# Kernel optimization log

Measured on AMD Instinct MI355X. Metric: run time of the kernel, lower is better.

## Reference

```python
import jax, jax.numpy as jnp
import numpy as np

EMBED = 1024
HEADS = 16
HEAD_DIM = EMBED // HEADS
WINDOW = 256

def _linear(x, W, b):
    # torch nn.Linear: y = x @ W.T + b, W shape (out, in)
    return jnp.einsum('bse,oe->bso', x, W) + b

def setup_inputs() -> dict:
    key = jax.random.key(0)
    ks = jax.random.split(key, 16)
    B, S = 2, 2048
    std = 1.0 / np.sqrt(EMBED)
    d = {
        'query': jax.random.normal(ks[0], (B, S, EMBED), jnp.float32),
        'key':   jax.random.normal(ks[1], (B, S, EMBED), jnp.float32),
        'value': jax.random.normal(ks[2], (B, S, EMBED), jnp.float32),
        'Wq': jax.random.normal(ks[3], (EMBED, EMBED), jnp.float32) * std,
        'bq': jnp.zeros((EMBED,), jnp.float32),
        'Wk': jax.random.normal(ks[4], (EMBED, EMBED), jnp.float32) * std,
        'bk': jnp.zeros((EMBED,), jnp.float32),
        'Wv': jax.random.normal(ks[5], (EMBED, EMBED), jnp.float32) * std,
        'bv': jnp.zeros((EMBED,), jnp.float32),
        'Wo': jax.random.normal(ks[6], (EMBED, EMBED), jnp.float32) * std,
        'bo': jnp.zeros((EMBED,), jnp.float32),
    }
    return d

def reference(query, key, value, Wq, bq, Wk, bk, Wv, bv, Wo, bo):
    B, S, E = query.shape
    q = _linear(query, Wq, bq)
    k = _linear(key, Wk, bk)
    v = _linear(value, Wv, bv)
    # (B, H, S, D)
    q = q.reshape(B, S, HEADS, HEAD_DIM).transpose(0, 2, 1, 3)
    k = k.reshape(B, S, HEADS, HEAD_DIM).transpose(0, 2, 1, 3)
    v = v.reshape(B, S, HEADS, HEAD_DIM).transpose(0, 2, 1, 3)
    scale = 1.0 / jnp.sqrt(jnp.asarray(HEAD_DIM, q.dtype))
    scores = jnp.einsum('bhqd,bhkd->bhqk', q, k) * scale
    # Faithful local masking: mask is 0 inside window [i-w//2, i+w//2], 1 outside,
    # and is ADDED to scores (as in the source, not -inf fill).
    i = jnp.arange(S)[:, None]
    j = jnp.arange(S)[None, :]
    half = WINDOW // 2
    band = (jnp.abs(i - j) <= half)
    add_mask = jnp.where(band, 0.0, 1.0).astype(scores.dtype)  # (S, S)
    scores = scores + add_mask[None, None, :, :]
    attn = jax.nn.softmax(scores, axis=-1)  # dropout = identity (eval)
    out = jnp.einsum('bhqk,bhkd->bhqd', attn, v)
    out = out.transpose(0, 2, 1, 3).reshape(B, S, E)
    return _linear(out, Wo, bo)
```

## Files before the change

kernel.cpp:

```cpp
#include <hip/hip_runtime.h>
#include <stdint.h>

#define B_ 2
#define S_ 2048
#define E_ 1024
#define H_ 16
#define D_ 64
#define M_ (B_*S_)
#define PROJ_ ((size_t)M_*E_)
#define HALF_W 128

typedef float    f32x4 __attribute__((ext_vector_type(4)));
typedef short    s16x4 __attribute__((ext_vector_type(4)));
typedef short    s16x8 __attribute__((ext_vector_type(8)));
typedef __bf16   bf16x8 __attribute__((ext_vector_type(8)));
typedef _Float16 f16x8 __attribute__((ext_vector_type(8)));
typedef unsigned int u32x4 __attribute__((ext_vector_type(4)));

typedef const __attribute__((address_space(1))) void* gas_t;
typedef __attribute__((address_space(3))) void*       las_t;

__device__ __forceinline__ void gl16(const void* g, void* l) {
    __builtin_amdgcn_global_load_lds((gas_t)g, (las_t)l, 16, 0, 0);
}

__device__ __forceinline__ f32x4 MFMA(bf16x8 a, bf16x8 b, f32x4 c) {
    return __builtin_amdgcn_mfma_f32_16x16x32_bf16(a, b, c, 0, 0, 0);
}
__device__ __forceinline__ f32x4 MFMAH(f16x8 a, f16x8 b, f32x4 c) {
    return __builtin_amdgcn_mfma_f32_16x16x32_f16(a, b, c, 0, 0, 0);
}

__device__ __forceinline__ float fexp2(float x) {
    return __builtin_amdgcn_exp2f(x);
}

__device__ __forceinline__ unsigned short f2bf(float f) {
    union { float f; unsigned int u; } x; x.f = f;
    unsigned int u = x.u + 0x7FFFu + ((x.u >> 16) & 1u);
    return (unsigned short)(u >> 16);
}

__device__ __forceinline__ s16x8 cvt8(f32x4 a, f32x4 b) {
    s16x8 h;
    h[0]=(short)f2bf(a[0]); h[1]=(short)f2bf(a[1]); h[2]=(short)f2bf(a[2]); h[3]=(short)f2bf(a[3]);
    h[4]=(short)f2bf(b[0]); h[5]=(short)f2bf(b[1]); h[6]=(short)f2bf(b[2]); h[7]=(short)f2bf(b[3]);
    return h;
}

__global__ __launch_bounds__(256) void cvt_kernel(
    const float* __restrict__ q, const float* __restrict__ k, const float* __restrict__ v,
    const float* __restrict__ Wq, const float* __restrict__ Wk,
    const float* __restrict__ Wv, const float* __restrict__ Wo,
    unsigned short* __restrict__ xq, unsigned short* __restrict__ xk,
    unsigned short* __restrict__ xv, unsigned short* __restrict__ wbf)
{
    const int z = blockIdx.y;
    if (z >= 3 && blockIdx.x >= 512) return;
    const float* src; unsigned short* dst;
    switch (z) {
        case 0: src = q;  dst = xq; break;
        case 1: src = k;  dst = xk; break;
        case 2: src = v;  dst = xv; break;
        case 3: src = Wq; dst = wbf; break;
        case 4: src = Wk; dst = wbf + (size_t)E_*E_; break;
        case 5: src = Wv; dst = wbf + 2*(size_t)E_*E_; break;
        default: src = Wo; dst = wbf + 3*(size_t)E_*E_; break;
    }
    size_t i = ((size_t)blockIdx.x * 256 + threadIdx.x) * 8;
    f32x4 a = *(const f32x4*)(src + i);
    f32x4 c = *(const f32x4*)(src + i + 4);
    *(s16x8*)(dst + i) = cvt8(a, c);
}

__global__ __launch_bounds__(256, 3) void qkv_kernel(
    const unsigned short* __restrict__ xq, const unsigned short* __restrict__ xk,
    const unsigned short* __restrict__ xv,
    const unsigned short* __restrict__ wbf,
    const float* __restrict__ Wq, const float* __restrict__ Wk, const float* __restrict__ Wv,
    const float* __restrict__ bq, const float* __restrict__ bk, const float* __restrict__ bv,
    unsigned short* __restrict__ qkvout)
{
    const int z = blockIdx.z;
    const unsigned short* X  = (z==0) ? xq : (z==1) ? xk : xv;
    const float*          Wf = (z==0) ? Wq : (z==1) ? Wk : Wv;
    const float*        bias = (z==0) ? bq : (z==1) ? bk : bv;
    const unsigned short* Wb = wbf ? (wbf + (size_t)z * E_ * E_) : nullptr;
    unsigned short* dst = qkvout + (size_t)z * PROJ_;

    __shared__ __align__(16) unsigned short As[2][128 * 32];
    __shared__ __align__(16) unsigned short Bs[2][128 * 32];

    const int t = threadIdx.x;
    const int lane = t & 63, w = t >> 6;
    const int quad = lane >> 4, l16 = lane & 15;
    const int wo = (w & 1) * 64, wsb = (w >> 1) * 64;
    const int oBase = blockIdx.x * 128, sBase = blockIdx.y * 128;

    const int r0 = t >> 2;
    const int c4 = (t & 3) ^ (r0 & 3);
    const unsigned short* gX  = X + (size_t)(sBase + r0) * E_ + c4 * 8;
    const unsigned short* gWb = Wb ? Wb + (size_t)(oBase + r0) * E_ + c4 * 8 : nullptr;
    const float*          gWf = Wf + (size_t)(oBase + r0) * E_ + c4 * 8;

    f32x4 acc[4][4] = {};

    auto issue = [&](int kk, int pb) {
        unsigned short* dB = &Bs[pb][(size_t)w * 512];
        gl16(gX + kk, dB);
        gl16(gX + (size_t)64 * E_ + kk, dB + 2048);
        if (gWb) {
            unsigned short* dA = &As[pb][(size_t)w * 512];
            gl16(gWb + kk, dA);
            gl16(gWb + (size_t)64 * E_ + kk, dA + 2048);
        } else {
            const float* gp0 = gWf + kk;
            const float* gp1 = gWf + (size_t)64 * E_ + kk;
            f32x4 a0 = *(const f32x4*)gp0, a1 = *(const f32x4*)(gp0 + 4);
            f32x4 b0 = *(const f32x4*)gp1, b1 = *(const f32x4*)(gp1 + 4);
            *(s16x8*)&As[pb][(size_t)r0 * 32 + (t & 3) * 8]        = cvt8(a0, a1);
            *(s16x8*)&As[pb][(size_t)(r0 + 64) * 32 + (t & 3) * 8] = cvt8(b0, b1);
        }
    };

    issue(0, 0);
    __syncthreads();

    for (int s = 0; s < 32; s++) {
        const int pb = s & 1;
        if (s < 31) issue((s + 1) * 32, pb ^ 1);

        bf16x8 af[4], bfr[4];
        #pragma unroll
        for (int io = 0; io < 4; io++) {
            int r = wo + io * 16 + l16;
            af[io] = *(const bf16x8*)&As[pb][(size_t)r * 32 + ((quad ^ (l16 & 3)) * 8)];
        }
        #pragma unroll
        for (int is = 0; is < 4; is++) {
            int r = wsb + is * 16 + l16;
            bfr[is] = *(const bf16x8*)&Bs[pb][(size_t)r * 32 + ((quad ^ (l16 & 3)) * 8)];
        }
        #pragma unroll
        for (int io = 0; io < 4; io++)
            #pragma unroll
            for (int is = 0; is < 4; is++)
                acc[io][is] = MFMA(af[io], bfr[is], acc[io][is]);
        __syncthreads();
    }

    const float KSCL = 0.1803368801111204f;
    #pragma unroll
    for (int is = 0; is < 4; is++) {
        int sg = sBase + wsb + is * 16 + l16;
        int b = sg >> 11, sg2 = sg & 2047;
        int k6 = sg2 & 63;
        int slot = ((k6 >> 5) & 1) * 32 + ((k6 >> 2) & 3) * 8
                 + ((k6 >> 4) & 1) * 4 + (k6 & 3);
        #pragma unroll
        for (int io = 0; io < 4; io++) {
            int ocol0 = oBase + wo + io * 16 + quad * 4;
            f32x4 bias4 = *(const f32x4*)&bias[ocol0];
            int h = ocol0 >> 6, d0 = ocol0 & 63;
            size_t base = ((size_t)(b * H_ + h)) * ((size_t)S_ * D_);
            if (z == 0) {
                s16x4 h4;
                #pragma unroll
                for (int r = 0; r < 4; r++) h4[r] = (short)f2bf(acc[io][is][r] + bias4[r]);
                *(s16x4*)&dst[base + (size_t)sg2 * D_ + d0] = h4;
            } else if (z == 1) {
                s16x4 h4;
                #pragma unroll
                for (int r = 0; r < 4; r++)
                    h4[r] = (short)f2bf((acc[io][is][r] + bias4[r]) * KSCL);
                *(s16x4*)&dst[base + (size_t)sg2 * D_ + d0] = h4;
            } else {
                size_t vb = base + (size_t)(sg2 >> 6) * 4096 + (size_t)d0 * 64 + slot;
                #pragma unroll
                for (int r = 0; r < 4; r++) {
                    _Float16 hv = (_Float16)(acc[io][is][r] + bias4[r]);
                    dst[vb + (size_t)r * 64] = __builtin_bit_cast(unsigned short, hv);
                }
            }
        }
    }
}

__global__ __launch_bounds__(256, 4) void attn_kernel(
    const unsigned short* __restrict__ qkvout, unsigned short* __restrict__ attnout)
{
    const int bh = blockIdx.x, b = bh >> 4, h = bh & 15;
    const int qbase = blockIdx.y * 64;
    const int t = threadIdx.x, w = t >> 6, lane = t & 63;
    const int quad = lane >> 4, l16 = lane & 15;

    const unsigned short* qg = qkvout + (size_t)bh * (S_ * D_);
    const unsigned short* kg = qkvout + PROJ_ + (size_t)bh * (S_ * D_);
    const unsigned short* vT = qkvout + 2 * PROJ_ + (size_t)bh * (S_ * D_);

    __shared__ __align__(16) unsigned short Ks [2][64 * 64];
    __shared__ __align__(16) unsigned short VTs[2][64 * 64];

    const int qi = qbase + w * 16 + l16;
    bf16x8 aq0 = *(const bf16x8*)&qg[(size_t)qi * 64 + quad * 8];
    bf16x8 aq1 = *(const bf16x8*)&qg[(size_t)qi * 64 + 32 + quad * 8];

    f32x4 Oi[4] = {}, Oo[4] = {};
    f32x4 Si = {}, So = {};

    const int r0 = t >> 3;
    const int ch = ((t & 7) ^ (r0 & 7)) * 8;

    f16x8 onesv;
    #pragma unroll
    for (int j = 0; j < 8; j++) onesv[j] = (_Float16)1.0f;

    auto issue = [&](int kt, int pb) {
        unsigned short* dK = &Ks [pb][(size_t)w * 512];
        unsigned short* dV = &VTs[pb][(size_t)w * 512];
        gl16(kg + (size_t)(kt + r0) * 64 + ch,      dK);
        gl16(kg + (size_t)(kt + r0 + 32) * 64 + ch, dK + 2048);
        gl16(vT + (size_t)(kt + r0) * 64 + ch,      dV);
        gl16(vT + (size_t)(kt + r0 + 32) * 64 + ch, dV + 2048);
    };

    issue(0, 0);
    __syncthreads();

    #pragma unroll 2
    for (int s = 0; s < 32; s++) {
        const int pb = s & 1;
        const int kt = s * 64;
        if (s < 31) issue(kt + 64, pb ^ 1);

        const int dq = qbase - kt;
        const int adq = dq < 0 ? -dq : dq;
        const int cls = (adq <= 64) ? 0 : (adq >= 192 ? 1 : 2);

        f32x4 pp[4];
        const int sw = l16 & 7;
        #pragma unroll
        for (int sub = 0; sub < 4; sub++) {
            int row = sub * 16 + l16;
            bf16x8 bk0 = *(const bf16x8*)&Ks[pb][(size_t)row * 64 + ((quad ^ sw) * 8)];
            bf16x8 bk1 = *(const bf16x8*)&Ks[pb][(size_t)row * 64 + (((4 + quad) ^ sw) * 8)];
            f32x4 zz = {};
            zz = MFMA(bk0, aq0, zz);
            zz = MFMA(bk1, aq1, zz);
            if (cls == 2) {
                const int jb = kt + sub * 16 + quad * 4;
                #pragma unroll
                for (int r = 0; r < 4; r++) {
                    int di = qi - (jb + r); di = di < 0 ? -di : di;
                    pp[sub][r] = fexp2(zz[r] + (di <= HALF_W ? 0.f : 1.44269504089f));
                }
            } else {
                #pragma unroll
                for (int r = 0; r < 4; r++) pp[sub][r] = fexp2(zz[r]);
            }
        }

        u32x4 u0, u1;
        u0[0] = __builtin_bit_cast(unsigned int, __builtin_amdgcn_cvt_pkrtz(pp[0][0], pp[0][1]));
        u0[1] = __builtin_bit_cast(unsigned int, __builtin_amdgcn_cvt_pkrtz(pp[0][2], pp[0][3]));
        u0[2] = __builtin_bit_cast(unsigned int, __builtin_amdgcn_cvt_pkrtz(pp[1][0], pp[1][1]));
        u0[3] = __builtin_bit_cast(unsigned int, __builtin_amdgcn_cvt_pkrtz(pp[1][2], pp[1][3]));
        u1[0] = __builtin_bit_cast(unsigned int, __builtin_amdgcn_cvt_pkrtz(pp[2][0], pp[2][1]));
        u1[1] = __builtin_bit_cast(unsigned int, __builtin_amdgcn_cvt_pkrtz(pp[2][2], pp[2][3]));
        u1[2] = __builtin_bit_cast(unsigned int, __builtin_amdgcn_cvt_pkrtz(pp[3][0], pp[3][1]));
        u1[3] = __builtin_bit_cast(unsigned int, __builtin_amdgcn_cvt_pkrtz(pp[3][2], pp[3][3]));
        f16x8 aP0 = __builtin_bit_cast(f16x8, u0);
        f16x8 aP1 = __builtin_bit_cast(f16x8, u1);

        if (cls == 1) {
            #pragma unroll
            for (int dt = 0; dt < 4; dt++) {
                int row = dt * 16 + l16;
                f16x8 v0 = *(const f16x8*)&VTs[pb][(size_t)row * 64 + ((quad ^ sw) * 8)];
                f16x8 v1 = *(const f16x8*)&VTs[pb][(size_t)row * 64 + (((4 + quad) ^ sw) * 8)];
                Oo[dt] = MFMAH(aP0, v0, Oo[dt]);
                Oo[dt] = MFMAH(aP1, v1, Oo[dt]);
            }
            So = MFMAH(aP0, onesv, So);
            So = MFMAH(aP1, onesv, So);
        } else {
            #pragma unroll
            for (int dt = 0; dt < 4; dt++) {
                int row = dt * 16 + l16;
                f16x8 v0 = *(const f16x8*)&VTs[pb][(size_t)row * 64 + ((quad ^ sw) * 8)];
                f16x8 v1 = *(const f16x8*)&VTs[pb][(size_t)row * 64 + (((4 + quad) ^ sw) * 8)];
                Oi[dt] = MFMAH(aP0, v0, Oi[dt]);
                Oi[dt] = MFMAH(aP1, v1, Oi[dt]);
            }
            Si = MFMAH(aP0, onesv, Si);
            Si = MFMAH(aP1, onesv, Si);
        }
        __syncthreads();
    }

    const float E1 = 2.718281828459045f;
    float rd[4];
    #pragma unroll
    for (int r = 0; r < 4; r++) rd[r] = 1.0f / (Si[r] + E1 * So[r]);
    #pragma unroll
    for (int dt = 0; dt < 4; dt++)
        #pragma unroll
        for (int r = 0; r < 4; r++) {
            float oo = (Oi[dt][r] + E1 * Oo[dt][r]) * rd[r];
            int srow2 = qbase + w * 16 + quad * 4 + r;
            int col   = h * 64 + dt * 16 + l16;
            attnout[((size_t)(b * S_ + srow2)) * E_ + col] = f2bf(oo);
        }
}

__global__ __launch_bounds__(256, 2) void oproj_kernel(
    const unsigned short* __restrict__ Aattn, const unsigned short* __restrict__ WoBf,
    const float* __restrict__ Wo, const float* __restrict__ bo, float* __restrict__ out)
{
    __shared__ __align__(16) unsigned short As[2][64 * 32];
    __shared__ __align__(16) unsigned short Bs[2][128 * 32];

    const int t = threadIdx.x;
    const int lane = t & 63, w = t >> 6;
    const int quad = lane >> 4, l16 = lane & 15;
    const int wm = (w & 1) * 32, wn = (w >> 1) * 64;
    const int rowBase = blockIdx.y * 64, nBase = blockIdx.x * 128;

    const int r0 = t >> 2;
    const int c4 = (t & 3) ^ (r0 & 3);
    const unsigned short* gA  = Aattn + (size_t)(rowBase + r0) * E_ + c4 * 8;
    const unsigned short* gBb = WoBf ? WoBf + (size_t)(nBase + r0) * E_ + c4 * 8 : nullptr;
    const float*          gBf = Wo + (size_t)(nBase + r0) * E_ + c4 * 8;

    f32x4 acc[2][4] = {};

    auto issue = [&](int kk, int pb) {
        gl16(gA + kk, &As[pb][(size_t)w * 512]);
        if (gBb) {
            unsigned short* dB = &Bs[pb][(size_t)w * 512];
            gl16(gBb + kk, dB);
            gl16(gBb + (size_t)64 * E_ + kk, dB + 2048);
        } else {
            const float* gp0 = gBf + kk;
            const float* gp1 = gBf + (size_t)64 * E_ + kk;
            f32x4 a0 = *(const f32x4*)gp0, a1 = *(const f32x4*)(gp0 + 4);
            f32x4 b0 = *(const f32x4*)gp1, b1 = *(const f32x4*)(gp1 + 4);
            *(s16x8*)&Bs[pb][(size_t)r0 * 32 + (t & 3) * 8]        = cvt8(a0, a1);
            *(s16x8*)&Bs[pb][(size_t)(r0 + 64) * 32 + (t & 3) * 8] = cvt8(b0, b1);
        }
    };

    issue(0, 0);
    __syncthreads();

    for (int s = 0; s < 32; s++) {
        const int pb = s & 1;
        if (s < 31) issue((s + 1) * 32, pb ^ 1);

        bf16x8 af[2], bfr[4];
        #pragma unroll
        for (int im = 0; im < 2; im++) {
            int r = wm + im * 16 + l16;
            af[im] = *(const bf16x8*)&As[pb][(size_t)r * 32 + ((quad ^ (l16 & 3)) * 8)];
        }
        #pragma unroll
        for (int in = 0; in < 4; in++) {
            int r = wn + in * 16 + l16;
            bfr[in] = *(const bf16x8*)&Bs[pb][(size_t)r * 32 + ((quad ^ (l16 & 3)) * 8)];
        }
        #pragma unroll
        for (int im = 0; im < 2; im++)
            #pragma unroll
            for (int in = 0; in < 4; in++)
                acc[im][in] = MFMA(af[im], bfr[in], acc[im][in]);
        __syncthreads();
    }

    #pragma unroll
    for (int im = 0; im < 2; im++)
      #pragma unroll
      for (int in = 0; in < 4; in++) {
          int col = nBase + wn + in * 16 + l16;
          float bb = bo[col];
          #pragma unroll
          for (int r = 0; r < 4; r++) {
              int row = rowBase + wm + im * 16 + quad * 4 + r;
              out[(size_t)row * E_ + col] = acc[im][in][r] + bb;
          }
      }
}

extern "C" void kernel_launch(void* const* d_in, const int* in_sizes, int n_in,
                              void* d_out, int out_size, void* d_ws, size_t ws_size,
                              hipStream_t stream) {
    const float* query = (const float*)d_in[0];
    const float* key_  = (const float*)d_in[1];
    const float* value = (const float*)d_in[2];
    const float* Wq = (const float*)d_in[3];
    const float* bq = (const float*)d_in[4];
    const float* Wk = (const float*)d_in[5];
    const float* bk = (const float*)d_in[6];
    const float* Wv = (const float*)d_in[7];
    const float* bv = (const float*)d_in[8];
    const float* Wo = (const float*)d_in[9];
    const float* bo = (const float*)d_in[10];

    unsigned short* ws      = (unsigned short*)d_ws;
    unsigned short* xv      = ws;
    unsigned short* attnout = ws;
    unsigned short* qkvout  = ws + PROJ_;
    size_t needW = (4 * PROJ_ + 4 * (size_t)E_ * E_) * 2;
    unsigned short* wbf = (ws_size >= needW) ? (ws + 4 * PROJ_) : nullptr;
    unsigned short* xq = (unsigned short*)d_out;
    unsigned short* xk = xq + PROJ_;

    cvt_kernel<<<dim3(2048, wbf ? 7 : 3), 256, 0, stream>>>(
        query, key_, value, Wq, Wk, Wv, Wo, xq, xk, xv, wbf);
    qkv_kernel<<<dim3(8, 32, 3), 256, 0, stream>>>(
        xq, xk, xv, wbf, Wq, Wk, Wv, bq, bk, bv, qkvout);
    attn_kernel<<<dim3(32, 32), 256, 0, stream>>>(qkvout, attnout);
    oproj_kernel<<<dim3(8, 64), 256, 0, stream>>>(
        attnout, wbf ? wbf + 3 * (size_t)E_ * E_ : nullptr, Wo, bo, (float*)d_out);
}
```

Measured before the change: 222.1 us.

## Process two query groups per wave to reuse K/V tiles, fold mask into MFMA accumulator

Each attention block now covers 128 query rows, with every wave handling two 16-row query groups, so each K/V tile staged in shared memory serves twice as many queries and the grid has half as many blocks. The additive mask is no longer kept as separate inside/outside accumulators combined with e at the end. It is seeded as the initial MFMA accumulator (0 or log2e) per element, leaving a single output and denominator accumulator. The cost is more registers, with launch bounds lowered to two blocks per SM, and fewer blocks in flight.

Result: slower. 226.7 us (+2.1%).

```diff
diff --git a/kernel.cpp b/kernel.cpp
--- a/kernel.cpp
+++ b/kernel.cpp
@@ -186,27 +186,32 @@
     }
 }
 
-__global__ __launch_bounds__(256, 4) void attn_kernel(
+__global__ __launch_bounds__(256, 2) void attn_kernel(
     const unsigned short* __restrict__ qkvout, unsigned short* __restrict__ attnout)
 {
     const int bh = blockIdx.x, b = bh >> 4, h = bh & 15;
-    const int qbase = blockIdx.y * 64;
+    const int qbase = blockIdx.y * 128;
     const int t = threadIdx.x, w = t >> 6, lane = t & 63;
     const int quad = lane >> 4, l16 = lane & 15;
 
-    const unsigned short* qg = qkvout + (size_t)bh * (S_ * D_);
+    const unsigned short* qgp = qkvout + (size_t)bh * (S_ * D_);
     const unsigned short* kg = qkvout + PROJ_ + (size_t)bh * (S_ * D_);
     const unsigned short* vT = qkvout + 2 * PROJ_ + (size_t)bh * (S_ * D_);
 
     __shared__ __align__(16) unsigned short Ks [2][64 * 64];
     __shared__ __align__(16) unsigned short VTs[2][64 * 64];
 
-    const int qi = qbase + w * 16 + l16;
-    bf16x8 aq0 = *(const bf16x8*)&qg[(size_t)qi * 64 + quad * 8];
-    bf16x8 aq1 = *(const bf16x8*)&qg[(size_t)qi * 64 + 32 + quad * 8];
-
-    f32x4 Oi[4] = {}, Oo[4] = {};
-    f32x4 Si = {}, So = {};
+    const int qw = qbase + w * 32;
+    bf16x8 aq[2][2];
+    #pragma unroll
+    for (int qg = 0; qg < 2; qg++) {
+        int qi = qw + qg * 16 + l16;
+        aq[qg][0] = *(const bf16x8*)&qgp[(size_t)qi * 64 + quad * 8];
+        aq[qg][1] = *(const bf16x8*)&qgp[(size_t)qi * 64 + 32 + quad * 8];
+    }
+
+    f32x4 O[2][4] = {};
+    f32x4 Sd[2] = {};
 
     const int r0 = t >> 3;
     const int ch = ((t & 7) ^ (r0 & 7)) * 8;
@@ -214,6 +219,10 @@
     f16x8 onesv;
     #pragma unroll
     for (int j = 0; j < 8; j++) onesv[j] = (_Float16)1.0f;
+
+    const float LOG2E = 1.44269504089f;
+    const f32x4 one4 = {LOG2E, LOG2E, LOG2E, LOG2E};
+    const f32x4 zero4 = {};
 
     auto issue = [&](int kt, int pb) {
         unsigned short* dK = &Ks [pb][(size_t)w * 512];
@@ -233,84 +242,86 @@
         const int kt = s * 64;
         if (s < 31) issue(kt + 64, pb ^ 1);
 
-        const int dq = qbase - kt;
-        const int adq = dq < 0 ? -dq : dq;
-        const int cls = (adq <= 64) ? 0 : (adq >= 192 ? 1 : 2);
-
-        f32x4 pp[4];
+        int cls[2];
+        #pragma unroll
+        for (int qg = 0; qg < 2; qg++) {
+            int d = qw + qg * 16 - kt;
+            cls[qg] = (d >= -64 && d <= 112) ? 0 : ((d >= 192 || d <= -144) ? 1 : 2);
+        }
+
         const int sw = l16 & 7;
+        u32x4 up[2][2];
         #pragma unroll
         for (int sub = 0; sub < 4; sub++) {
             int row = sub * 16 + l16;
             bf16x8 bk0 = *(const bf16x8*)&Ks[pb][(size_t)row * 64 + ((quad ^ sw) * 8)];
             bf16x8 bk1 = *(const bf16x8*)&Ks[pb][(size_t)row * 64 + (((4 + quad) ^ sw) * 8)];
-            f32x4 zz = {};
-            zz = MFMA(bk0, aq0, zz);
-            zz = MFMA(bk1, aq1, zz);
-            if (cls == 2) {
-                const int jb = kt + sub * 16 + quad * 4;
-                #pragma unroll
-                for (int r = 0; r < 4; r++) {
-                    int di = qi - (jb + r); di = di < 0 ? -di : di;
-                    pp[sub][r] = fexp2(zz[r] + (di <= HALF_W ? 0.f : 1.44269504089f));
+            #pragma unroll
+            for (int qg = 0; qg < 2; qg++) {
+                f32x4 ci;
+                if (cls[qg] == 0) {
+                    ci = zero4;
+                } else if (cls[qg] == 1) {
+                    ci = one4;
+                } else {
+                    int jb = kt + sub * 16 + quad * 4;
+                    int qi = qw + qg * 16 + l16;
+                    #pragma unroll
+                    for (int r = 0; r < 4; r++) {
+                        int di = qi - (jb + r); di = di < 0 ? -di : di;
+                        ci[r] = (di <= HALF_W) ? 0.f : LOG2E;
+                    }
                 }
-            } else {
-                #pragma unroll
-                for (int r = 0; r < 4; r++) pp[sub][r] = fexp2(zz[r]);
+                f32x4 zz = MFMA(bk0, aq[qg][0], ci);
+                zz = MFMA(bk1, aq[qg][1], zz);
+                float p0 = fexp2(zz[0]), p1 = fexp2(zz[1]);
+                float p2 = fexp2(zz[2]), p3 = fexp2(zz[3]);
+                up[qg][sub >> 1][(sub & 1) * 2 + 0] =
+                    __builtin_bit_cast(unsigned int, __builtin_amdgcn_cvt_pkrtz(p0, p1));
+                up[qg][sub >> 1][(sub & 1) * 2 + 1] =
+                    __builtin_bit_cast(unsigned int, __builtin_amdgcn_cvt_pkrtz(p2, p3));
             }
         }
-
-        u32x4 u0, u1;
-        u0[0] = __builtin_bit_cast(unsigned int, __builtin_amdgcn_cvt_pkrtz(pp[0][0], pp[0][1]));
-        u0[1] = __builtin_bit_cast(unsigned int, __builtin_amdgcn_cvt_pkrtz(pp[0][2], pp[0][3]));
-        u0[2] = __builtin_bit_cast(unsigned int, __builtin_amdgcn_cvt_pkrtz(pp[1][0], pp[1][1]));
-        u0[3] = __builtin_bit_cast(unsigned int, __builtin_amdgcn_cvt_pkrtz(pp[1][2], pp[1][3]));
-        u1[0] = __builtin_bit_cast(unsigned int, __builtin_amdgcn_cvt_pkrtz(pp[2][0], pp[2][1]));
-        u1[1] = __builtin_bit_cast(unsigned int, __builtin_amdgcn_cvt_pkrtz(pp[2][2], pp[2][3]));
-        u1[2] = __builtin_bit_cast(unsigned int, __builtin_amdgcn_cvt_pkrtz(pp[3][0], pp[3][1]));
-        u1[3] = __builtin_bit_cast(unsigned int, __builtin_amdgcn_cvt_pkrtz(pp[3][2], pp[3][3]));
-        f16x8 aP0 = __builtin_bit_cast(f16x8, u0);
-        f16x8 aP1 = __builtin_bit_cast(f16x8, u1);
-
-        if (cls == 1) {
+        f16x8 aP[2][2];
+        aP[0][0] = __builtin_bit_cast(f16x8, up[0][0]);
+        aP[0][1] = __builtin_bit_cast(f16x8, up[0][1]);
+        aP[1][0] = __builtin_bit_cast(f16x8, up[1][0]);
+        aP[1][1] = __builtin_bit_cast(f16x8, up[1][1]);
+
+        #pragma unroll
+        for (int dt = 0; dt < 4; dt++) {
+            int row = dt * 16 + l16;
+            f16x8 v0 = *(const f16x8*)&VTs[pb][(size_t)row * 64 + ((quad ^ sw) * 8)];
+            f16x8 v1 = *(const f16x8*)&VTs[pb][(size_t)row * 64 + (((4 + quad) ^ sw) * 8)];
             #pragma unroll
-            for (int dt = 0; dt < 4; dt++) {
-                int row = dt * 16 + l16;
-                f16x8 v0 = *(const f16x8*)&VTs[pb][(size_t)row * 64 + ((quad ^ sw) * 8)];
-                f16x8 v1 = *(const f16x8*)&VTs[pb][(size_t)row * 64 + (((4 + quad) ^ sw) * 8)];
-                Oo[dt] = MFMAH(aP0, v0, Oo[dt]);
-                Oo[dt] = MFMAH(aP1, v1, Oo[dt]);
+            for (int qg = 0; qg < 2; qg++) {
+                O[qg][dt] = MFMAH(aP[qg][0], v0, O[qg][dt]);
+                O[qg][dt] = MFMAH(aP[qg][1], v1, O[qg][dt]);
             }
-            So = MFMAH(aP0, onesv, So);
-            So = MFMAH(aP1, onesv, So);
-        } else {
+        }
+        #pragma unroll
+        for (int qg = 0; qg < 2; qg++) {
+            Sd[qg] = MFMAH(aP[qg][0], onesv, Sd[qg]);
+            Sd[qg] = MFMAH(aP[qg][1], onesv, Sd[qg]);
+        }
+        __syncthreads();
+    }
+
+    #pragma unroll
+    for (int qg = 0; qg < 2; qg++) {
+        float rd[4];
+        #pragma unroll
+        for (int r = 0; r < 4; r++) rd[r] = 1.0f / Sd[qg][r];
+        #pragma unroll
+        for (int dt = 0; dt < 4; dt++)
             #pragma unroll
-            for (int dt = 0; dt < 4; dt++) {
-                int row = dt * 16 + l16;
-                f16x8 v0 = *(const f16x8*)&VTs[pb][(size_t)row * 64 + ((quad ^ sw) * 8)];
-                f16x8 v1 = *(const f16x8*)&VTs[pb][(size_t)row * 64 + (((4 + quad) ^ sw) * 8)];
-                Oi[dt] = MFMAH(aP0, v0, Oi[dt]);
-                Oi[dt] = MFMAH(aP1, v1, Oi[dt]);
+            for (int r = 0; r < 4; r++) {
+                float oo = O[qg][dt][r] * rd[r];
+                int srow2 = qw + qg * 16 + quad * 4 + r;
+                int col   = h * 64 + dt * 16 + l16;
+                attnout[((size_t)(b * S_ + srow2)) * E_ + col] = f2bf(oo);
             }
-            Si = MFMAH(aP0, onesv, Si);
-            Si = MFMAH(aP1, onesv, Si);
-        }
-        __syncthreads();
-    }
-
-    const float E1 = 2.718281828459045f;
-    float rd[4];
-    #pragma unroll
-    for (int r = 0; r < 4; r++) rd[r] = 1.0f / (Si[r] + E1 * So[r]);
-    #pragma unroll
-    for (int dt = 0; dt < 4; dt++)
-        #pragma unroll
-        for (int r = 0; r < 4; r++) {
-            float oo = (Oi[dt][r] + E1 * Oo[dt][r]) * rd[r];
-            int srow2 = qbase + w * 16 + quad * 4 + r;
-            int col   = h * 64 + dt * 16 + l16;
-            attnout[((size_t)(b * S_ + srow2)) * E_ + col] = f2bf(oo);
-        }
+    }
 }
 
 __global__ __launch_bounds__(256, 2) void oproj_kernel(
@@ -418,7 +429,7 @@
         query, key_, value, Wq, Wk, Wv, Wo, xq, xk, xv, wbf);
     qkv_kernel<<<dim3(8, 32, 3), 256, 0, stream>>>(
         xq, xk, xv, wbf, Wq, Wk, Wv, bq, bk, bv, qkvout);
-    attn_kernel<<<dim3(32, 32), 256, 0, stream>>>(qkvout, attnout);
+    attn_kernel<<<dim3(32, 16), 256, 0, stream>>>(qkvout, attnout);
     oproj_kernel<<<dim3(8, 64), 256, 0, stream>>>(
         attnout, wbf ? wbf + 3 * (size_t)E_ * E_ : nullptr, Wo, bo, (float*)d_out);
 }
```
